# Kernel tuning notes

Measured on AMD Instinct MI355X. Metric: run time of the kernel, lower is better.

## Reference

```python
import jax, jax.numpy as jnp
import numpy as np

B, S, IN_DIM, P_DIM, H = 2, 2048, 1024, 512, 8
HD = P_DIM // H
N_PENTA = 1024
SCALES = (128, 256, 512)
K_NEIGH = max(16, min(int(S * 0.15), 128))  # adaptive window -> 128
SCALE = 1.0 / float(np.sqrt(HD))
EPS = 1e-5


def _ln(x, g, b):
    mu = jnp.mean(x, axis=-1, keepdims=True)
    var = jnp.mean((x - mu) ** 2, axis=-1, keepdims=True)
    return (x - mu) * jax.lax.rsqrt(var + EPS) * g + b


def setup_inputs() -> dict:
    key = jax.random.key(0)
    ks = list(jax.random.split(key, 6 + 2 * len(SCALES)))
    w = lambda k, shp: jax.random.normal(k, shp, jnp.float32) * 0.02
    inp = {
        'sequence_features': jax.random.normal(ks[0], (B, S, IN_DIM), jnp.float32),
        'shared_pentachora': jax.random.normal(ks[1], (N_PENTA, 5, P_DIM), jnp.float32),
        'shared_positions': jax.random.uniform(ks[2], (N_PENTA,), dtype=jnp.float32),
        'proj_W': w(ks[3], (IN_DIM, P_DIM)), 'proj_b': jnp.zeros((P_DIM,), jnp.float32),
        'ln_g': jnp.ones((P_DIM,), jnp.float32), 'ln_b': jnp.zeros((P_DIM,), jnp.float32),
        'qkv_W': w(ks[4], (P_DIM, 3 * P_DIM)), 'qkv_b': jnp.zeros((3 * P_DIM,), jnp.float32),
        'out_W': w(ks[5], (P_DIM, P_DIM)), 'out_b': jnp.zeros((P_DIM,), jnp.float32),
    }
    i = 6
    for s in SCALES:
        inp[f'w1_{s}'] = w(ks[i], (P_DIM, 2 * s)); inp[f'b1_{s}'] = jnp.zeros((2 * s,), jnp.float32)
        inp[f'g_{s}'] = jnp.ones((2 * s,), jnp.float32); inp[f'bb_{s}'] = jnp.zeros((2 * s,), jnp.float32)
        inp[f'w2_{s}'] = w(ks[i + 1], (2 * s, s)); inp[f'b2_{s}'] = jnp.zeros((s,), jnp.float32)
        i += 2
    return inp


def _attend_one(z_b, pos_b, qkv_W, qkv_b, out_W, out_b):
    # z_b: [S, P_DIM], pos_b: [S]
    qkv = (z_b @ qkv_W + qkv_b).reshape(S, 3, H, HD)
    q = jnp.transpose(qkv[:, 0], (1, 0, 2))  # [H, S, HD]
    k = jnp.transpose(qkv[:, 1], (1, 0, 2))
    v = jnp.transpose(qkv[:, 2], (1, 0, 2))
    dist = jnp.abs(pos_b[:, None] - pos_b[None, :])  # [S, S]
    _, routes = jax.lax.top_k(-dist, K_NEIGH)        # [S, K] nearest in Cantor space
    kg = k[:, routes, :]  # [H, S, K, HD] gathered keys
    vg = v[:, routes, :]
    scores = jnp.einsum('hqd,hqkd->hqk', q, kg) * SCALE
    attn = jax.nn.softmax(scores, axis=-1)
    out = jnp.einsum('hqk,hqkd->hqd', attn, vg)
    out = jnp.transpose(out, (1, 0, 2)).reshape(S, P_DIM)
    return out @ out_W + out_b


def reference(sequence_features, shared_pentachora, shared_positions, proj_W, proj_b, ln_g, ln_b, qkv_W, qkv_b, out_W, out_b, w1_128, b1_128, g_128, bb_128, w2_128, b2_128, w1_256, b1_256, g_256, bb_256, w2_256, b2_256, w1_512, b1_512, g_512, bb_512, w2_512, b2_512):
    # centroids from pentachora vertices, L2-normalized
    cent = shared_pentachora.mean(axis=1)
    cent = cent / jnp.clip(jnp.linalg.norm(cent, axis=-1, keepdims=True), 1e-12)
    # input projection -> LN -> GELU -> L2 normalize
    z = jax.nn.gelu(_ln(sequence_features @ proj_W + proj_b, ln_g, ln_b), approximate=False)
    z = z / jnp.clip(jnp.linalg.norm(z, axis=-1, keepdims=True), 1e-12)
    # match to opinion anchors, inherit Cantor positions
    anchor_ids = jnp.argmax(jnp.einsum('bnd,pd->bnp', z, cent), axis=-1)  # [B, S]
    cantor_positions = shared_positions[anchor_ids]  # [B, S]
    # per-sample geometric sparse attention (vmapped over batch)
    z_att = jax.vmap(_attend_one, in_axes=(0, 0, None, None, None, None))(
        z, cantor_positions, qkv_W, qkv_b, out_W, out_b)  # [B, S, P_DIM]
    pooled = z_att.mean(axis=1)  # [B, P_DIM] (no attention mask)
    scale_params = (
        (w1_128, b1_128, g_128, bb_128, w2_128, b2_128),
        (w1_256, b1_256, g_256, bb_256, w2_256, b2_256),
        (w1_512, b1_512, g_512, bb_512, w2_512, b2_512),
    )
    outs = []
    for (w1, b1, g, bb, w2, b2) in scale_params:
        h = jax.nn.gelu(_ln(pooled @ w1 + b1, g, bb), approximate=False)
        outs.append(h @ w2 + b2)
    return jnp.concatenate(outs, axis=-1)  # [B, 128+256+512] concatenated scale opinions
```

## Files before the change

kernel.cpp:

```cpp
#include <hip/hip_runtime.h>
#include <math.h>

#define DEV __device__ __forceinline__

static constexpr int S_LEN  = 2048;
static constexpr int IN_DIM = 1024;
static constexpr int P_DIM  = 512;
static constexpr int NHEAD  = 8;
static constexpr int HD     = 64;
static constexpr int KN     = 128;

typedef __attribute__((ext_vector_type(8))) short bf16x8;
typedef __attribute__((ext_vector_type(4))) float f32x4;

DEV float gelu_exact(float x) {
    return 0.5f * x * (1.0f + erff(x * 0.70710678118654752440f));
}

DEV short bf_hi(float x) {
    unsigned u = __float_as_uint(x);
    unsigned r = (u + 0x7fffu + ((u >> 16) & 1u)) >> 16;
    return (short)r;
}
DEV float bf_f(short h) { return __uint_as_float(((unsigned)(unsigned short)h) << 16); }

DEV float block_reduce_sum(float v, float* sm4) {
    #pragma unroll
    for (int off = 32; off; off >>= 1) v += __shfl_down(v, off, 64);
    int lane = threadIdx.x & 63, w = threadIdx.x >> 6;
    __syncthreads();
    if (lane == 0) sm4[w] = v;
    __syncthreads();
    return sm4[0] + sm4[1] + sm4[2] + sm4[3];
}

__global__ __launch_bounds__(256) void k_cent(const float* __restrict__ penta,
                                              short* __restrict__ ch,
                                              short* __restrict__ cl) {
    int p = blockIdx.x, t = threadIdx.x;
    __shared__ float sm4[4];
    float c0 = 0.f, c1 = 0.f;
    #pragma unroll
    for (int v = 0; v < 5; v++) {
        const float* row = penta + ((long)p * 5 + v) * P_DIM;
        c0 += row[t];
        c1 += row[t + 256];
    }
    c0 /= 5.0f; c1 /= 5.0f;
    float tot = block_reduce_sum(c0 * c0 + c1 * c1, sm4);
    float n = fmaxf(sqrtf(tot), 1e-12f);
    float v0 = c0 / n, v1 = c1 / n;
    short h0 = bf_hi(v0), h1 = bf_hi(v1);
    ch[p * P_DIM + t]       = h0;
    ch[p * P_DIM + t + 256] = h1;
    cl[p * P_DIM + t]       = bf_hi(v0 - bf_f(h0));
    cl[p * P_DIM + t + 256] = bf_hi(v1 - bf_f(h1));
}

template <int K, int N>
__global__ __launch_bounds__(256) void k_wt(const float* __restrict__ W,
                                            short* __restrict__ WTh,
                                            short* __restrict__ WTl) {
    __shared__ float tile[64][65];
    int bk = blockIdx.x, bn = blockIdx.y;
    int t = threadIdx.x;
    int c = t & 63, r4 = t >> 6;
    #pragma unroll
    for (int i = 0; i < 16; i++) {
        int row = r4 + i * 4;
        tile[row][c] = W[(long)(bk * 64 + row) * N + bn * 64 + c];
    }
    __syncthreads();
    #pragma unroll
    for (int i = 0; i < 16; i++) {
        int n = r4 + i * 4;
        float v = tile[c][n];
        short h = bf_hi(v);
        long o = (long)(bn * 64 + n) * K + bk * 64 + c;
        WTh[o] = h;
        WTl[o] = bf_hi(v - bf_f(h));
    }
}

template <int BM, int K, int N, int EPI, bool SPLITA>
__global__ __launch_bounds__(256) void k_mm(const float* __restrict__ Af,
                                            const short* __restrict__ Ash,
                                            const short* __restrict__ Asl,
                                            const short* __restrict__ BTh,
                                            const short* __restrict__ BTl,
                                            const float* __restrict__ bias,
                                            float* __restrict__ C,
                                            unsigned long long* __restrict__ rowkey) {
    constexpr int TI = BM / 32;
    __shared__ short Ah[BM * 40], Al[BM * 40], Bh[128 * 40], Bl[128 * 40];
    int t = threadIdx.x;
    int lane = t & 63, wave = t >> 6;
    int wr = (wave >> 1) * (BM / 2), wc = (wave & 1) * 64;
    int m = lane & 15, quad = lane >> 4;
    int rb = blockIdx.x * BM, cb = blockIdx.y * 128;

    f32x4 acc[TI][4];
    #pragma unroll
    for (int i = 0; i < TI; i++)
        #pragma unroll
        for (int j = 0; j < 4; j++) acc[i][j] = (f32x4){0.f, 0.f, 0.f, 0.f};

    for (int k0 = 0; k0 < K; k0 += 32) {
        __syncthreads();
        if constexpr (SPLITA) {
            #pragma unroll
            for (int ps = 0; ps < BM / 64; ps++) {
                int idx = t + ps * 256;
                int row = idx >> 2, c4 = idx & 3;
                *(float4*)(Ah + row * 40 + c4 * 8) =
                    *(const float4*)(Ash + (long)(rb + row) * K + k0 + c4 * 8);
                *(float4*)(Al + row * 40 + c4 * 8) =
                    *(const float4*)(Asl + (long)(rb + row) * K + k0 + c4 * 8);
            }
        } else {
            #pragma unroll
            for (int ps = 0; ps < BM / 32; ps++) {
                int row = (t >> 3) + ps * 32;
                int seg = t & 7;
                float4 v = *(const float4*)(Af + (long)(rb + row) * K + k0 + seg * 4);
                short h0 = bf_hi(v.x), h1 = bf_hi(v.y), h2 = bf_hi(v.z), h3 = bf_hi(v.w);
                short l0 = bf_hi(v.x - bf_f(h0)), l1 = bf_hi(v.y - bf_f(h1));
                short l2 = bf_hi(v.z - bf_f(h2)), l3 = bf_hi(v.w - bf_f(h3));
                *(short4*)(Ah + row * 40 + seg * 4) = make_short4(h0, h1, h2, h3);
                *(short4*)(Al + row * 40 + seg * 4) = make_short4(l0, l1, l2, l3);
            }
        }
        #pragma unroll
        for (int ps = 0; ps < 2; ps++) {
            int row = (t >> 2) + ps * 64;
            int seg = t & 3;
            *(float4*)(Bh + row * 40 + seg * 8) =
                *(const float4*)(BTh + (long)(cb + row) * K + k0 + seg * 8);
            *(float4*)(Bl + row * 40 + seg * 8) =
                *(const float4*)(BTl + (long)(cb + row) * K + k0 + seg * 8);
        }
        __syncthreads();

        bf16x8 ah[TI], al[TI], bh[4], bl[4];
        #pragma unroll
        for (int i = 0; i < TI; i++) {
            ah[i] = *(const bf16x8*)(Ah + (wr + i * 16 + m) * 40 + quad * 8);
            al[i] = *(const bf16x8*)(Al + (wr + i * 16 + m) * 40 + quad * 8);
        }
        #pragma unroll
        for (int j = 0; j < 4; j++) {
            bh[j] = *(const bf16x8*)(Bh + (wc + j * 16 + m) * 40 + quad * 8);
            bl[j] = *(const bf16x8*)(Bl + (wc + j * 16 + m) * 40 + quad * 8);
        }
        #pragma unroll
        for (int i = 0; i < TI; i++)
            #pragma unroll
            for (int j = 0; j < 4; j++) {
                acc[i][j] = __builtin_amdgcn_mfma_f32_16x16x32_bf16(ah[i], bh[j], acc[i][j], 0, 0, 0);
                acc[i][j] = __builtin_amdgcn_mfma_f32_16x16x32_bf16(ah[i], bl[j], acc[i][j], 0, 0, 0);
                acc[i][j] = __builtin_amdgcn_mfma_f32_16x16x32_bf16(al[i], bh[j], acc[i][j], 0, 0, 0);
            }
    }

    if (EPI == 0) {
        #pragma unroll
        for (int i = 0; i < TI; i++) {
            int gr0 = rb + wr + i * 16 + quad * 4;
            #pragma unroll
            for (int j = 0; j < 4; j++) {
                int gc = cb + wc + j * 16 + m;
                float bv = bias[gc];
                #pragma unroll
                for (int r = 0; r < 4; r++)
                    C[(long)(gr0 + r) * N + gc] = acc[i][j][r] + bv;
            }
        }
    } else {
        #pragma unroll
        for (int i = 0; i < TI; i++) {
            #pragma unroll
            for (int r = 0; r < 4; r++) {
                int gr = rb + wr + i * 16 + quad * 4 + r;
                float bv = acc[i][0][r];
                int bp = cb + wc + m;
                #pragma unroll
                for (int j = 1; j < 4; j++) {
                    float v = acc[i][j][r];
                    int p = cb + wc + j * 16 + m;
                    if (v > bv) { bv = v; bp = p; }
                }
                #pragma unroll
                for (int off = 1; off < 16; off <<= 1) {
                    float ov = __shfl_xor(bv, off, 64);
                    int op = __shfl_xor(bp, off, 64);
                    if (ov > bv || (ov == bv && op < bp)) { bv = ov; bp = op; }
                }
                if (m == 0) {
                    unsigned u = __float_as_uint(bv);
                    u = (u & 0x80000000u) ? ~u : (u | 0x80000000u);
                    unsigned long long key =
                        ((unsigned long long)u << 32) | (unsigned)(0xFFFFFFFFu - (unsigned)bp);
                    atomicMax(&rowkey[gr], key);
                }
            }
        }
    }
}

__global__ __launch_bounds__(256) void k_ln_gelu_norm(const float* __restrict__ Zin,
                                                      const float* __restrict__ g,
                                                      const float* __restrict__ b,
                                                      short* __restrict__ z_h,
                                                      short* __restrict__ z_l) {
    long row = blockIdx.x;
    int t = threadIdx.x;
    __shared__ float sm4[4];
    float x0 = Zin[row * P_DIM + t], x1 = Zin[row * P_DIM + t + 256];
    float mu = block_reduce_sum(x0 + x1, sm4) * (1.0f / P_DIM);
    float d0 = x0 - mu, d1 = x1 - mu;
    float var = block_reduce_sum(d0 * d0 + d1 * d1, sm4) * (1.0f / P_DIM);
    float rs = 1.0f / sqrtf(var + 1e-5f);
    float y0 = gelu_exact(d0 * rs * g[t] + b[t]);
    float y1 = gelu_exact(d1 * rs * g[t + 256] + b[t + 256]);
    float nn = block_reduce_sum(y0 * y0 + y1 * y1, sm4);
    float n = fmaxf(sqrtf(nn), 1e-12f);
    float v0 = y0 / n, v1 = y1 / n;
    short h0 = bf_hi(v0), h1 = bf_hi(v1);
    z_h[row * P_DIM + t]       = h0;
    z_h[row * P_DIM + t + 256] = h1;
    z_l[row * P_DIM + t]       = bf_hi(v0 - bf_f(h0));
    z_l[row * P_DIM + t + 256] = bf_hi(v1 - bf_f(h1));
}

__global__ __launch_bounds__(256) void k_sort(const unsigned long long* __restrict__ rowkey,
                                              const float* __restrict__ spos,
                                              int* __restrict__ order,
                                              float* __restrict__ pos_srt) {
    int b = blockIdx.x, t = threadIdx.x;
    __shared__ unsigned long long key[2048];
    for (int u = 0; u < 8; u++) {
        int i = t + u * 256;
        unsigned p = 0xFFFFFFFFu - (unsigned)(rowkey[b * 2048 + i] & 0xFFFFFFFFull);
        float pv = spos[p];
        key[i] = (((unsigned long long)__float_as_uint(pv)) << 32) | (unsigned)i;
    }
    __syncthreads();
    for (int k = 2; k <= 2048; k <<= 1) {
        for (int j = k >> 1; j > 0; j >>= 1) {
            for (int u = 0; u < 8; u++) {
                int i = t + u * 256;
                int l = i ^ j;
                if (l > i) {
                    bool up = ((i & k) == 0);
                    unsigned long long a = key[i], c = key[l];
                    if ((a > c) == up) { key[i] = c; key[l] = a; }
                }
            }
            __syncthreads();
        }
    }
    for (int u = 0; u < 8; u++) {
        int r = t + u * 256;
        unsigned long long kk = key[r];
        order[b * 2048 + r]   = (int)(kk & 0xffffffffu);
        pos_srt[b * 2048 + r] = __uint_as_float((unsigned)(kk >> 32));
    }
}

__global__ __launch_bounds__(256) void k_routes(const float* __restrict__ pos_srt,
                                                const int* __restrict__ order,
                                                unsigned long long* __restrict__ bmG,
                                                uint2* __restrict__ bounds) {
    int blk = blockIdx.x;
    int b = blk >> 9;
    int t = threadIdx.x;
    int lane = t & 63, wave = t >> 6;
    int r = (blk & 511) * 4 + wave;
    __shared__ float ps[2048];
    __shared__ unsigned short tk[2048];
    for (int u = 0; u < 8; u++) {
        int i = t + u * 256;
        ps[i] = pos_srt[b * 2048 + i];
        tk[i] = (unsigned short)order[b * 2048 + i];
    }
    __syncthreads();

    float pi = ps[r];
    float T = 3e38f;
    #pragma unroll
    for (int a2 = 0; a2 < 2; a2++) {
        int a = lane + a2 * 64;
        int jl = r - a, jr = r + 127 - a;
        if (jl >= 0 && jr <= 2047) {
            float dl = (a > 0)   ? (pi - ps[jl]) : 0.f;
            float dr = (a < 127) ? (ps[jr] - pi) : 0.f;
            T = fminf(T, fmaxf(dl, dr));
        }
    }
    #pragma unroll
    for (int off = 1; off < 64; off <<= 1) T = fminf(T, __shfl_xor(T, off, 64));

    int lo = 0, hi = r;
    while (lo < hi) { int mid = (lo + hi) >> 1; if (pi - ps[mid] <= T) hi = mid; else lo = mid + 1; }
    int mn = lo;
    lo = r; hi = 2047;
    while (lo < hi) { int mid = (lo + hi + 1) >> 1; if (ps[mid] - pi <= T) lo = mid; else hi = mid - 1; }
    int mx = lo;
    int Ls, Rs;
    if (T > 0.f) {
        lo = 0; hi = r;
        while (lo < hi) { int mid = (lo + hi) >> 1; if (pi - ps[mid] < T) hi = mid; else lo = mid + 1; }
        Ls = lo;
        lo = r; hi = 2047;
        while (lo < hi) { int mid = (lo + hi + 1) >> 1; if (ps[mid] - pi < T) lo = mid; else hi = mid - 1; }
        Rs = lo;
    } else { Ls = r + 1; Rs = r - 1; }

    int cnt_strict = (Rs >= Ls) ? (Rs - Ls + 1) : 0;
    int need = 128 - cnt_strict;
    int l0a, l0b, r0a, r0b;
    if (cnt_strict > 0) { l0a = mn; l0b = Ls - 1; r0a = Rs + 1; r0b = mx; }
    else                { l0a = mn; l0b = mx;     r0a = 1;      r0b = 0; }
    int nL = (l0b >= l0a) ? (l0b - l0a + 1) : 0;
    int nR = (r0b >= r0a) ? (r0b - r0a + 1) : 0;
    int tiecount = nL + nR;

    int X = 65535;
    if (need < tiecount) {
        int lo2 = 0, hi2 = 2047;
        while (lo2 < hi2) {
            int mid = (lo2 + hi2) >> 1;
            int cnt = 0;
            for (int e = lane; e < tiecount; e += 64) {
                int j = (e < nL) ? (l0a + e) : (r0a + e - nL);
                cnt += (tk[j] <= mid) ? 1 : 0;
            }
            #pragma unroll
            for (int off = 1; off < 64; off <<= 1) cnt += __shfl_xor(cnt, off, 64);
            if (cnt >= need) hi2 = mid; else lo2 = mid + 1;
        }
        X = lo2;
    }

    int qlo_loc = 1 << 30, qhi_loc = -1;
    if (lane < 32) {
        unsigned long long bits = 0;
        int j0 = lane << 6, j1 = j0 + 63;
        if (cnt_strict > 0) {
            int a0 = max(Ls, j0), a1 = min(Rs, j1);
            if (a0 <= a1) {
                int s = a0 - j0, e = a1 - j0;
                unsigned long long msk = (e - s == 63) ? ~0ull
                                       : (((1ull << (e - s + 1)) - 1) << s);
                bits |= msk;
            }
        }
        int a0 = max(l0a, j0), a1 = min(l0b, j1);
        for (int j = a0; j <= a1; j++) if (tk[j] <= X) bits |= 1ull << (j - j0);
        a0 = max(r0a, j0); a1 = min(r0b, j1);
        for (int j = a0; j <= a1; j++) if (tk[j] <= X) bits |= 1ull << (j - j0);
        if (bits) {
            qlo_loc = j0 + __builtin_ctzll(bits);
            qhi_loc = j0 + 63 - __builtin_clzll(bits);
        }
        bmG[((long)(b * 2048 + r)) * 32 + lane] = bits;
    }
    #pragma unroll
    for (int off = 1; off < 64; off <<= 1) {
        qlo_loc = min(qlo_loc, __shfl_xor(qlo_loc, off, 64));
        qhi_loc = max(qhi_loc, __shfl_xor(qhi_loc, off, 64));
    }
    if (lane == 0)
        bounds[b * 2048 + r] = make_uint2((unsigned)qlo_loc, (unsigned)qhi_loc);
}

__global__ __launch_bounds__(256) void k_attn(const float* __restrict__ qkv,
                                              const int* __restrict__ order,
                                              const unsigned long long* __restrict__ bmG,
                                              const uint2* __restrict__ bounds,
                                              short* __restrict__ attn_h,
                                              short* __restrict__ attn_l) {
    __shared__ __align__(16) char smem[72320];
    short* Khi = (short*)smem;
    short* Klo = (short*)(smem + 17408);
    short* Vt  = (short*)(smem + 34816);
    short* Pt  = (short*)(smem + 57344);
    unsigned short* cm = (unsigned short*)(smem + 67584);
    int* sh_tok = (int*)(smem + 71680);
    int* sh_lohi = (int*)(smem + 71744);
    float2* ml = (float2*)(smem + 71752);
    float* Opart = (float*)smem;

    int gb = blockIdx.x;
    int b  = gb >> 9;
    int qg = (gb >> 2) & 127;
    int hp = gb & 3;
    int h0 = hp * 2;
    int r0 = qg * 16;
    int t = threadIdx.x;
    int lane = t & 63, wave = t >> 6;
    int rh = wave & 1, hs = wave >> 1;
    int key = lane & 15, quad = lane >> 4;

    const float4* qkvF4 = (const float4*)qkv;

    if (t < 16) sh_tok[t] = order[b * 2048 + r0 + t];
    if (t == 0) { sh_lohi[0] = 1 << 30; sh_lohi[1] = 0; }
    #pragma unroll
    for (int u = 0; u < 8; u++) {
        int e = t + u * 256;
        int c = e >> 4, q = e & 15;
        cm[c * 16 + q] = (unsigned short)(
            (bmG[((long)(b * 2048 + r0 + q)) * 32 + (c >> 2)] >> ((c & 3) * 16)) & 0xFFFF);
    }
    __syncthreads();
    if (t < 16) {
        uint2 bd = bounds[b * 2048 + r0 + t];
        atomicMin(&sh_lohi[0], (int)bd.x);
        atomicMax(&sh_lohi[1], (int)bd.y);
    }

    bf16x8 qh[2], ql[2];
    {
        long tq = (long)(b * 2048 + sh_tok[key]) * 384;
        #pragma unroll
        for (int ks = 0; ks < 2; ks++) {
            float4 v0 = qkvF4[tq + (h0 + hs) * 16 + ks * 8 + quad * 2];
            float4 v1 = qkvF4[tq + (h0 + hs) * 16 + ks * 8 + quad * 2 + 1];
            float vv[8] = {v0.x, v0.y, v0.z, v0.w, v1.x, v1.y, v1.z, v1.w};
            #pragma unroll
            for (int j = 0; j < 8; j++) {
                short hb = bf_hi(vv[j]);
                qh[ks][j] = hb;
                ql[ks][j] = bf_hi(vv[j] - bf_f(hb));
            }
        }
    }
    __syncthreads();
    int lo = sh_lohi[0] & ~63, hi = sh_lohi[1] + 1;

    float mrow[4], lrow[4];
    f32x4 Ont[4];
    #pragma unroll
    for (int r = 0; r < 4; r++) { mrow[r] = -1e30f; lrow[r] = 0.f; }
    #pragma unroll
    for (int nt = 0; nt < 4; nt++) Ont[nt] = (f32x4){0.f, 0.f, 0.f, 0.f};

    short* PtH = Pt + wave * 1280;
    short* PtL = PtH + 640;

    for (int c0 = lo; c0 < hi; c0 += 64) {
        __syncthreads();
        #pragma unroll
        for (int u = 0; u < 8; u++) {
            int idx = t + u * 256;
            int rl = idx >> 5, f4p = idx & 31;
            int rank = c0 + rl;
            int tok = order[b * 2048 + min(rank, 2047)];
            float4 v = qkvF4[(long)(b * 2048 + tok) * 384 + 128 + h0 * 16 + f4p];
            short h0s = bf_hi(v.x), h1s = bf_hi(v.y), h2s = bf_hi(v.z), h3s = bf_hi(v.w);
            *(short4*)(Khi + rl * 136 + f4p * 4) = make_short4(h0s, h1s, h2s, h3s);
            *(short4*)(Klo + rl * 136 + f4p * 4) =
                make_short4(bf_hi(v.x - bf_f(h0s)), bf_hi(v.y - bf_f(h1s)),
                            bf_hi(v.z - bf_f(h2s)), bf_hi(v.w - bf_f(h3s)));
        }
        {
            int rq = t & 15;
            int dp = t >> 4;
            float4 va[4][2];
            #pragma unroll
            for (int i = 0; i < 4; i++) {
                int rank = c0 + rq * 4 + i;
                int tok = order[b * 2048 + min(rank, 2047)];
                long base = (long)(b * 2048 + tok) * 384 + 256 + h0 * 16 + dp * 2;
                va[i][0] = qkvF4[base];
                va[i][1] = qkvF4[base + 1];
            }
            #pragma unroll
            for (int j2 = 0; j2 < 2; j2++)
                #pragma unroll
                for (int c = 0; c < 4; c++) {
                    const float* f0 = (const float*)&va[0][j2];
                    const float* f1 = (const float*)&va[1][j2];
                    const float* f2 = (const float*)&va[2][j2];
                    const float* f3 = (const float*)&va[3][j2];
                    *(short4*)(Vt + (dp * 8 + j2 * 4 + c) * 88 + rq * 4) =
                        make_short4(bf_hi(f0[c]), bf_hi(f1[c]), bf_hi(f2[c]), bf_hi(f3[c]));
                }
        }
        __syncthreads();

        int cb = c0 + rh * 32;
        if (cb >= hi) continue;
        int ch0 = cb >> 4;
        unsigned long long m0 = *(const unsigned long long*)(cm + ch0 * 16 + quad * 4);
        unsigned long long m1 = (ch0 + 1 < 128)
            ? *(const unsigned long long*)(cm + (ch0 + 1) * 16 + quad * 4) : 0ull;
        if (!__any((m0 | m1) != 0ull)) continue;

        f32x4 S0 = (f32x4){0.f,0.f,0.f,0.f}, S1 = (f32x4){0.f,0.f,0.f,0.f};
        #pragma unroll
        for (int ks = 0; ks < 2; ks++) {
            const short* kb0 = Khi + (rh * 32 + key) * 136 + hs * 64 + ks * 32 + quad * 8;
            const short* kl0 = Klo + (rh * 32 + key) * 136 + hs * 64 + ks * 32 + quad * 8;
            const short* kb1 = kb0 + 16 * 136;
            const short* kl1 = kl0 + 16 * 136;
            bf16x8 b0h = *(const bf16x8*)kb0, b0l = *(const bf16x8*)kl0;
            bf16x8 b1h = *(const bf16x8*)kb1, b1l = *(const bf16x8*)kl1;
            S0 = __builtin_amdgcn_mfma_f32_16x16x32_bf16(qh[ks], b0h, S0, 0, 0, 0);
            S0 = __builtin_amdgcn_mfma_f32_16x16x32_bf16(qh[ks], b0l, S0, 0, 0, 0);
            S0 = __builtin_amdgcn_mfma_f32_16x16x32_bf16(ql[ks], b0h, S0, 0, 0, 0);
            S1 = __builtin_amdgcn_mfma_f32_16x16x32_bf16(qh[ks], b1h, S1, 0, 0, 0);
            S1 = __builtin_amdgcn_mfma_f32_16x16x32_bf16(qh[ks], b1l, S1, 0, 0, 0);
            S1 = __builtin_amdgcn_mfma_f32_16x16x32_bf16(ql[ks], b1h, S1, 0, 0, 0);
        }
        float s0[4], s1[4], p0[4], p1[4];
        unsigned bit0[4], bit1[4];
        #pragma unroll
        for (int r = 0; r < 4; r++) {
            bit0[r] = (unsigned)((m0 >> (r * 16 + key)) & 1);
            bit1[r] = (unsigned)((m1 >> (r * 16 + key)) & 1);
            s0[r] = bit0[r] ? S0[r] * 0.125f : -1e30f;
            s1[r] = bit1[r] ? S1[r] * 0.125f : -1e30f;
        }
        #pragma unroll
        for (int r = 0; r < 4; r++) {
            float cmax = fmaxf(s0[r], s1[r]);
            cmax = fmaxf(cmax, __shfl_xor(cmax, 1, 64));
            cmax = fmaxf(cmax, __shfl_xor(cmax, 2, 64));
            cmax = fmaxf(cmax, __shfl_xor(cmax, 4, 64));
            cmax = fmaxf(cmax, __shfl_xor(cmax, 8, 64));
            float mn = fmaxf(mrow[r], cmax);
            float alpha = __expf(mrow[r] - mn);
            mrow[r] = mn;
            p0[r] = bit0[r] ? __expf(s0[r] - mn) : 0.f;
            p1[r] = bit1[r] ? __expf(s1[r] - mn) : 0.f;
            float rs = p0[r] + p1[r];
            rs += __shfl_xor(rs, 1, 64);
            rs += __shfl_xor(rs, 2, 64);
            rs += __shfl_xor(rs, 4, 64);
            rs += __shfl_xor(rs, 8, 64);
            lrow[r] = lrow[r] * alpha + rs;
            #pragma unroll
            for (int nt = 0; nt < 4; nt++) Ont[nt][r] *= alpha;
        }
        #pragma unroll
        for (int r = 0; r < 4; r++) {
            short ha = bf_hi(p0[r]);
            PtH[(quad * 4 + r) * 40 + key] = ha;
            PtL[(quad * 4 + r) * 40 + key] = bf_hi(p0[r] - bf_f(ha));
            short hb = bf_hi(p1[r]);
            PtH[(quad * 4 + r) * 40 + 16 + key] = hb;
            PtL[(quad * 4 + r) * 40 + 16 + key] = bf_hi(p1[r] - bf_f(hb));
        }
        bf16x8 pfh = *(const bf16x8*)(PtH + key * 40 + quad * 8);
        bf16x8 pfl = *(const bf16x8*)(PtL + key * 40 + quad * 8);
        #pragma unroll
        for (int nt = 0; nt < 4; nt++) {
            bf16x8 vf = *(const bf16x8*)(Vt + (hs * 64 + nt * 16 + key) * 88
                                         + rh * 32 + quad * 8);
            Ont[nt] = __builtin_amdgcn_mfma_f32_16x16x32_bf16(pfh, vf, Ont[nt], 0, 0, 0);
            Ont[nt] = __builtin_amdgcn_mfma_f32_16x16x32_bf16(pfl, vf, Ont[nt], 0, 0, 0);
        }
    }

    if (key == 0) {
        #pragma unroll
        for (int r = 0; r < 4; r++)
            ml[(rh * 2 + hs) * 16 + quad * 4 + r] = make_float2(mrow[r], lrow[r]);
    }
    __syncthreads();
    #pragma unroll
    for (int nt = 0; nt < 4; nt++)
        #pragma unroll
        for (int r = 0; r < 4; r++)
            Opart[rh * 2048 + (quad * 4 + r) * 128 + hs * 64 + nt * 16 + key] = Ont[nt][r];
    __syncthreads();

    {
        int q = t >> 4, hs2 = (t >> 3) & 1, ds = t & 7;
        float2 a = ml[(0 * 2 + hs2) * 16 + q];
        float2 c = ml[(1 * 2 + hs2) * 16 + q];
        float M = fmaxf(a.x, c.x);
        float w0 = __expf(a.x - M), w1 = __expf(c.x - M);
        float denom = a.y * w0 + c.y * w1;
        float inv = 1.0f / fmaxf(denom, 1e-37f);
        long off = (long)(b * 2048 + sh_tok[q]) * P_DIM + (h0 + hs2) * HD + ds * 8;
        short hsv[8], lsv[8];
        #pragma unroll
        for (int j = 0; j < 8; j++) {
            int d = hs2 * 64 + ds * 8 + j;
            float o = (Opart[q * 128 + d] * w0 + Opart[2048 + q * 128 + d] * w1) * inv;
            hsv[j] = bf_hi(o);
            lsv[j] = bf_hi(o - bf_f(hsv[j]));
        }
        *(short4*)(attn_h + off)     = make_short4(hsv[0], hsv[1], hsv[2], hsv[3]);
        *(short4*)(attn_h + off + 4) = make_short4(hsv[4], hsv[5], hsv[6], hsv[7]);
        *(short4*)(attn_l + off)     = make_short4(lsv[0], lsv[1], lsv[2], lsv[3]);
        *(short4*)(attn_l + off + 4) = make_short4(lsv[4], lsv[5], lsv[6], lsv[7]);
    }
}

__global__ __launch_bounds__(256) void k_pool(const float* __restrict__ zatt,
                                              float* __restrict__ pooled) {
    int b = blockIdx.y, chunk = blockIdx.x, t = threadIdx.x;
    float a0 = 0.f, a1 = 0.f;
    for (int s = 0; s < 16; s++) {
        long row = ((long)b * S_LEN + chunk * 16 + s) * P_DIM;
        a0 += zatt[row + t];
        a1 += zatt[row + t + 256];
    }
    atomicAdd(&pooled[b * P_DIM + t], a0);
    atomicAdd(&pooled[b * P_DIM + t + 256], a1);
}

__global__ __launch_bounds__(256) void k_exp_fc1(const float* __restrict__ pooled,
                                                 const float* __restrict__ w1_0, const float* __restrict__ b1_0,
                                                 const float* __restrict__ w1_1, const float* __restrict__ b1_1,
                                                 const float* __restrict__ w1_2, const float* __restrict__ b1_2,
                                                 float* __restrict__ h) {
    int t = threadIdx.x, b = blockIdx.y;
    int c = blockIdx.x * 256 + t;
    __shared__ float pl[P_DIM];
    pl[t]       = pooled[b * P_DIM + t]       * (1.0f / S_LEN);
    pl[t + 256] = pooled[b * P_DIM + t + 256] * (1.0f / S_LEN);
    __syncthreads();

    const float* wp; const float* bp; int s2, j;
    if (c < 256)      { wp = w1_0; bp = b1_0; s2 = 256;  j = c; }
    else if (c < 768) { wp = w1_1; bp = b1_1; s2 = 512;  j = c - 256; }
    else              { wp = w1_2; bp = b1_2; s2 = 1024; j = c - 768; }

    const float* p = wp + j;
    float acc = 0.f;
    #pragma unroll 16
    for (int k = 0; k < P_DIM; k++) {
        acc = fmaf(pl[k], *p, acc);
        p += s2;
    }
    h[(long)b * 1792 + c] = acc + bp[j];
}

__global__ __launch_bounds__(256) void k_exp_ln(float* __restrict__ h,
                                                const float* __restrict__ g0, const float* __restrict__ bb0,
                                                const float* __restrict__ g1, const float* __restrict__ bb1,
                                                const float* __restrict__ g2, const float* __restrict__ bb2) {
    int e = blockIdx.x, b = blockIdx.y, t = threadIdx.x;
    __shared__ float sm4[4];
    const int offs[3] = {0, 256, 768};
    const int ns[3]   = {256, 512, 1024};
    const float* gs[3]  = {g0, g1, g2};
    const float* bbs[3] = {bb0, bb1, bb2};
    int n = ns[e];
    float* hp = h + (long)b * 1792 + offs[e];
    const float* g = gs[e]; const float* bb = bbs[e];

    float x[4];
    float loc = 0.f;
    for (int u = 0; u < 4; u++) {
        int j = t + u * 256;
        x[u] = (j < n) ? hp[j] : 0.f;
        loc += x[u];
    }
    float mu = block_reduce_sum(loc, sm4) / (float)n;
    loc = 0.f;
    for (int u = 0; u < 4; u++) {
        int j = t + u * 256;
        if (j < n) { float d = x[u] - mu; loc += d * d; }
    }
    float var = block_reduce_sum(loc, sm4) / (float)n;
    float rs = 1.0f / sqrtf(var + 1e-5f);
    for (int u = 0; u < 4; u++) {
        int j = t + u * 256;
        if (j < n) hp[j] = gelu_exact((x[u] - mu) * rs * g[j] + bb[j]);
    }
}

__global__ __launch_bounds__(256) void k_exp_fc2(const float* __restrict__ h,
                                                 const float* __restrict__ w2_0, const float* __restrict__ b2_0,
                                                 const float* __restrict__ w2_1, const float* __restrict__ b2_1,
                                                 const float* __restrict__ w2_2, const float* __restrict__ b2_2,
                                                 float* __restrict__ out) {
    int t = threadIdx.x, b = blockIdx.y;
    int c = blockIdx.x * 256 + t;
    __shared__ float hs[1792];
    for (int u = 0; u < 7; u++) hs[t + u * 256] = h[(long)b * 1792 + t + u * 256];
    __syncthreads();
    if (c >= 896) return;

    const float* wp; const float* bp; int s2, sN, j, off_h;
    if (c < 128)      { wp = w2_0; bp = b2_0; s2 = 256;  sN = 128; j = c;       off_h = 0; }
    else if (c < 384) { wp = w2_1; bp = b2_1; s2 = 512;  sN = 256; j = c - 128; off_h = 256; }
    else              { wp = w2_2; bp = b2_2; s2 = 1024; sN = 512; j = c - 384; off_h = 768; }

    const float* p = wp + j;
    const float* hh = hs + off_h;
    float acc = 0.f;
    #pragma unroll 16
    for (int k = 0; k < s2; k++) {
        acc = fmaf(hh[k], *p, acc);
        p += sN;
    }
    out[b * 896 + c] = acc + bp[j];
}

extern "C" void kernel_launch(void* const* d_in, const int* in_sizes, int n_in,
                              void* d_out, int out_size, void* d_ws, size_t ws_size,
                              hipStream_t stream) {
    const float* seq   = (const float*)d_in[0];
    const float* penta = (const float*)d_in[1];
    const float* spos  = (const float*)d_in[2];
    const float* projW = (const float*)d_in[3];
    const float* projb = (const float*)d_in[4];
    const float* lng   = (const float*)d_in[5];
    const float* lnb   = (const float*)d_in[6];
    const float* qkvW  = (const float*)d_in[7];
    const float* qkvb  = (const float*)d_in[8];
    const float* outW  = (const float*)d_in[9];
    const float* outb  = (const float*)d_in[10];

    float* ws      = (float*)d_ws;
    float* z_pre   = ws;
    short* z_h     = (short*)(z_pre + 2097152);
    short* z_l     = z_h + 2097152;
    float* qkv     = (float*)(z_l + 2097152);
    float* pos     = qkv + 6291456;
    float* pooled  = pos + 4096;
    float* hbuf    = pooled + 1024;
    unsigned long long* rowkey = (unsigned long long*)(hbuf + 4096);
    float* pos_srt = (float*)(rowkey + 4096);
    int*   order   = (int*)(pos_srt + 4096);
    uint2* bounds  = (uint2*)(order + 4096);
    unsigned long long* bmG = (unsigned long long*)(bounds + 4096);
    short* cent_h  = (short*)(bmG + 131072);
    short* cent_l  = cent_h + 524288;
    short* pjWT_h  = cent_l + 524288;
    short* pjWT_l  = pjWT_h + 524288;
    short* qkWT_h  = pjWT_l + 524288;
    short* qkWT_l  = qkWT_h + 786432;
    short* owWT_h  = qkWT_l + 786432;
    short* owWT_l  = owWT_h + 262144;
    short* attn_h  = z_h;
    short* attn_l  = z_l;
    float* zatt    = z_pre;

    k_cent<<<1024, 256, 0, stream>>>(penta, cent_h, cent_l);
    { dim3 g(16, 8);  k_wt<IN_DIM, P_DIM><<<g, 256, 0, stream>>>(projW, pjWT_h, pjWT_l); }
    { dim3 g(8, 24);  k_wt<P_DIM, 3 * P_DIM><<<g, 256, 0, stream>>>(qkvW, qkWT_h, qkWT_l); }
    { dim3 g(8, 8);   k_wt<P_DIM, P_DIM><<<g, 256, 0, stream>>>(outW, owWT_h, owWT_l); }

    { dim3 g(64, 4);  k_mm<64, IN_DIM, P_DIM, 0, false><<<g, 256, 0, stream>>>(
          seq, nullptr, nullptr, pjWT_h, pjWT_l, projb, z_pre, nullptr); }
    k_ln_gelu_norm<<<4096, 256, 0, stream>>>(z_pre, lng, lnb, z_h, z_l);

    hipMemsetAsync(rowkey, 0, 4096 * sizeof(unsigned long long), stream);
    { dim3 g(64, 8);  k_mm<64, P_DIM, 1024, 1, true><<<g, 256, 0, stream>>>(
          nullptr, z_h, z_l, cent_h, cent_l, nullptr, nullptr, rowkey); }
    k_sort<<<2, 256, 0, stream>>>(rowkey, spos, order, pos_srt);

    { dim3 g(64, 12); k_mm<64, P_DIM, 3 * P_DIM, 0, true><<<g, 256, 0, stream>>>(
          nullptr, z_h, z_l, qkWT_h, qkWT_l, qkvb, qkv, nullptr); }
    k_routes<<<1024, 256, 0, stream>>>(pos_srt, order, bmG, bounds);
    k_attn<<<1024, 256, 0, stream>>>(qkv, order, bmG, bounds, attn_h, attn_l);
    { dim3 g(64, 4);  k_mm<64, P_DIM, P_DIM, 0, true><<<g, 256, 0, stream>>>(
          nullptr, attn_h, attn_l, owWT_h, owWT_l, outb, zatt, nullptr); }

    hipMemsetAsync(pooled, 0, 1024 * sizeof(float), stream);
    { dim3 pg(128, 2); k_pool<<<pg, 256, 0, stream>>>(zatt, pooled); }

    dim3 g1(7, 2);
    k_exp_fc1<<<g1, 256, 0, stream>>>(pooled,
        (const float*)d_in[11], (const float*)d_in[12],
        (const float*)d_in[17], (const float*)d_in[18],
        (const float*)d_in[23], (const float*)d_in[24], hbuf);
    dim3 g2(3, 2);
    k_exp_ln<<<g2, 256, 0, stream>>>(hbuf,
        (const float*)d_in[13], (const float*)d_in[14],
        (const float*)d_in[19], (const float*)d_in[20],
        (const float*)d_in[25], (const float*)d_in[26]);
    dim3 g3(4, 2);
    k_exp_fc2<<<g3, 256, 0, stream>>>(hbuf,
        (const float*)d_in[15], (const float*)d_in[16],
        (const float*)d_in[21], (const float*)d_in[22],
        (const float*)d_in[27], (const float*)d_in[28], (float*)d_out);
}
```

Before: 403.4 us.

## Pre-sort and pre-split K/V into global bf16 layouts before attention

Two new kernels gather K and V in sorted Cantor order once. K is split into bf16 hi/lo halves and V is transposed to bf16 in global scratch buffers. The attention kernel then reads MFMA fragments straight from global memory instead of re-gathering and converting K/V into LDS for every query block. This removes redundant conversion work and two syncthreads per chunk, and shrinks LDS use to allow more occupancy. The cost is extra kernel launches, scratch traffic, and uncoalesced global fragment loads inside the inner loop that rely on cache hits.

```diff
diff --git a/kernel.cpp b/kernel.cpp
--- a/kernel.cpp
+++ b/kernel.cpp
@@ -374,22 +374,75 @@
         bounds[b * 2048 + r] = make_uint2((unsigned)qlo_loc, (unsigned)qhi_loc);
 }
 
+__global__ __launch_bounds__(256) void k_kprep(const float* __restrict__ qkv,
+                                               const int* __restrict__ order,
+                                               short* __restrict__ Ks_h,
+                                               short* __restrict__ Ks_l) {
+    int b = blockIdx.y;
+    int t = threadIdx.x;
+    int lr = t >> 5;
+    int seg = t & 31;
+    int rank = blockIdx.x * 8 + lr;
+    int tok = order[b * 2048 + rank];
+    const float4* src = (const float4*)qkv + (long)(b * 2048 + tok) * 384 + 128 + seg * 4;
+    long dsto = (long)(b * 2048 + rank) * 512 + seg * 16;
+    #pragma unroll
+    for (int u = 0; u < 4; u++) {
+        float4 v = src[u];
+        short h0 = bf_hi(v.x), h1 = bf_hi(v.y), h2 = bf_hi(v.z), h3 = bf_hi(v.w);
+        *(short4*)(Ks_h + dsto + u * 4) = make_short4(h0, h1, h2, h3);
+        *(short4*)(Ks_l + dsto + u * 4) =
+            make_short4(bf_hi(v.x - bf_f(h0)), bf_hi(v.y - bf_f(h1)),
+                        bf_hi(v.z - bf_f(h2)), bf_hi(v.w - bf_f(h3)));
+    }
+}
+
+__global__ __launch_bounds__(256) void k_vprep(const float* __restrict__ qkv,
+                                               const int* __restrict__ order,
+                                               short* __restrict__ Vt_h) {
+    __shared__ short tile[64][72];
+    int rt = blockIdx.x, dt = blockIdx.y, b = blockIdx.z;
+    int t = threadIdx.x;
+    int lr = t >> 2;
+    int q4 = t & 3;
+    int tok = order[b * 2048 + rt * 64 + lr];
+    const float4* src = (const float4*)qkv + (long)(b * 2048 + tok) * 384 + 256 + dt * 16;
+    #pragma unroll
+    for (int u = 0; u < 4; u++) {
+        float4 v = src[q4 + u * 4];
+        int d0 = (q4 + u * 4) * 4;
+        tile[d0 + 0][lr] = bf_hi(v.x);
+        tile[d0 + 1][lr] = bf_hi(v.y);
+        tile[d0 + 2][lr] = bf_hi(v.z);
+        tile[d0 + 3][lr] = bf_hi(v.w);
+    }
+    __syncthreads();
+    int d = t >> 2, c4 = t & 3;
+    long o = ((long)(b * 512 + dt * 64 + d)) * 2048 + rt * 64 + c4 * 16;
+    #pragma unroll
+    for (int j = 0; j < 4; j++)
+        *(short4*)(Vt_h + o + j * 4) = make_short4(tile[d][c4 * 16 + j * 4 + 0],
+                                                   tile[d][c4 * 16 + j * 4 + 1],
+                                                   tile[d][c4 * 16 + j * 4 + 2],
+                                                   tile[d][c4 * 16 + j * 4 + 3]);
+}
+
 __global__ __launch_bounds__(256) void k_attn(const float* __restrict__ qkv,
                                               const int* __restrict__ order,
                                               const unsigned long long* __restrict__ bmG,
                                               const uint2* __restrict__ bounds,
+                                              const short* __restrict__ Ks_h,
+                                              const short* __restrict__ Ks_l,
+                                              const short* __restrict__ Vt_h,
                                               short* __restrict__ attn_h,
                                               short* __restrict__ attn_l) {
-    __shared__ __align__(16) char smem[72320];
-    short* Khi = (short*)smem;
-    short* Klo = (short*)(smem + 17408);
-    short* Vt  = (short*)(smem + 34816);
-    short* Pt  = (short*)(smem + 57344);
-    unsigned short* cm = (unsigned short*)(smem + 67584);
-    int* sh_tok = (int*)(smem + 71680);
-    int* sh_lohi = (int*)(smem + 71744);
-    float2* ml = (float2*)(smem + 71752);
+    __shared__ __align__(16) char smem[17024];
+    short* Pt = (short*)smem;
+    unsigned short* cm = (unsigned short*)(smem + 10240);
     float* Opart = (float*)smem;
+    float2* ml = (float2*)(smem + 16384);
+    int* sh_tok = (int*)(smem + 16896);
+    int* sh_lohi = (int*)(smem + 16960);
 
     int gb = blockIdx.x;
     int b  = gb >> 9;
@@ -449,47 +502,11 @@
     short* PtH = Pt + wave * 1280;
     short* PtL = PtH + 640;
 
+    int hd = h0 + hs;
+    long kbase = ((long)b * 2048) * 512 + hd * 64 + quad * 8;
+    long vbase = ((long)(b * 512 + hd * 64 + key)) * 2048;
+
     for (int c0 = lo; c0 < hi; c0 += 64) {
-        __syncthreads();
-        #pragma unroll
-        for (int u = 0; u < 8; u++) {
-            int idx = t + u * 256;
-            int rl = idx >> 5, f4p = idx & 31;
-            int rank = c0 + rl;
-            int tok = order[b * 2048 + min(rank, 2047)];
-            float4 v = qkvF4[(long)(b * 2048 + tok) * 384 + 128 + h0 * 16 + f4p];
-            short h0s = bf_hi(v.x), h1s = bf_hi(v.y), h2s = bf_hi(v.z), h3s = bf_hi(v.w);
-            *(short4*)(Khi + rl * 136 + f4p * 4) = make_short4(h0s, h1s, h2s, h3s);
-            *(short4*)(Klo + rl * 136 + f4p * 4) =
-                make_short4(bf_hi(v.x - bf_f(h0s)), bf_hi(v.y - bf_f(h1s)),
-                            bf_hi(v.z - bf_f(h2s)), bf_hi(v.w - bf_f(h3s)));
-        }
-        {
-            int rq = t & 15;
-            int dp = t >> 4;
-            float4 va[4][2];
-            #pragma unroll
-            for (int i = 0; i < 4; i++) {
-                int rank = c0 + rq * 4 + i;
-                int tok = order[b * 2048 + min(rank, 2047)];
-                long base = (long)(b * 2048 + tok) * 384 + 256 + h0 * 16 + dp * 2;
-                va[i][0] = qkvF4[base];
-                va[i][1] = qkvF4[base + 1];
-            }
-            #pragma unroll
-            for (int j2 = 0; j2 < 2; j2++)
-                #pragma unroll
-                for (int c = 0; c < 4; c++) {
-                    const float* f0 = (const float*)&va[0][j2];
-                    const float* f1 = (const float*)&va[1][j2];
-                    const float* f2 = (const float*)&va[2][j2];
-                    const float* f3 = (const float*)&va[3][j2];
-                    *(short4*)(Vt + (dp * 8 + j2 * 4 + c) * 88 + rq * 4) =
-                        make_short4(bf_hi(f0[c]), bf_hi(f1[c]), bf_hi(f2[c]), bf_hi(f3[c]));
-                }
-        }
-        __syncthreads();
-
         int cb = c0 + rh * 32;
         if (cb >= hi) continue;
         int ch0 = cb >> 4;
@@ -498,15 +515,16 @@
             ? *(const unsigned long long*)(cm + (ch0 + 1) * 16 + quad * 4) : 0ull;
         if (!__any((m0 | m1) != 0ull)) continue;
 
+        long kr0 = kbase + (long)(cb + key) * 512;
+        long kr1 = kbase + (long)(cb + 16 + key) * 512;
+
         f32x4 S0 = (f32x4){0.f,0.f,0.f,0.f}, S1 = (f32x4){0.f,0.f,0.f,0.f};
         #pragma unroll
         for (int ks = 0; ks < 2; ks++) {
-            const short* kb0 = Khi + (rh * 32 + key) * 136 + hs * 64 + ks * 32 + quad * 8;
-            const short* kl0 = Klo + (rh * 32 + key) * 136 + hs * 64 + ks * 32 + quad * 8;
-            const short* kb1 = kb0 + 16 * 136;
-            const short* kl1 = kl0 + 16 * 136;
-            bf16x8 b0h = *(const bf16x8*)kb0, b0l = *(const bf16x8*)kl0;
-            bf16x8 b1h = *(const bf16x8*)kb1, b1l = *(const bf16x8*)kl1;
+            bf16x8 b0h = *(const bf16x8*)(Ks_h + kr0 + ks * 32);
+            bf16x8 b0l = *(const bf16x8*)(Ks_l + kr0 + ks * 32);
+            bf16x8 b1h = *(const bf16x8*)(Ks_h + kr1 + ks * 32);
+            bf16x8 b1l = *(const bf16x8*)(Ks_l + kr1 + ks * 32);
             S0 = __builtin_amdgcn_mfma_f32_16x16x32_bf16(qh[ks], b0h, S0, 0, 0, 0);
             S0 = __builtin_amdgcn_mfma_f32_16x16x32_bf16(qh[ks], b0l, S0, 0, 0, 0);
             S0 = __builtin_amdgcn_mfma_f32_16x16x32_bf16(ql[ks], b0h, S0, 0, 0, 0);
@@ -557,8 +575,8 @@
         bf16x8 pfl = *(const bf16x8*)(PtL + key * 40 + quad * 8);
         #pragma unroll
         for (int nt = 0; nt < 4; nt++) {
-            bf16x8 vf = *(const bf16x8*)(Vt + (hs * 64 + nt * 16 + key) * 88
-                                         + rh * 32 + quad * 8);
+            bf16x8 vf = *(const bf16x8*)(Vt_h + vbase + (long)nt * 16 * 2048
+                                         + cb + quad * 8);
             Ont[nt] = __builtin_amdgcn_mfma_f32_16x16x32_bf16(pfh, vf, Ont[nt], 0, 0, 0);
             Ont[nt] = __builtin_amdgcn_mfma_f32_16x16x32_bf16(pfl, vf, Ont[nt], 0, 0, 0);
         }
@@ -744,6 +762,10 @@
     short* attn_l  = z_l;
     float* zatt    = z_pre;
 
+    short* Ks_h = (short*)z_pre;
+    short* Ks_l = Ks_h + 2097152;
+    short* Vt_h = cent_h;
+
     k_cent<<<1024, 256, 0, stream>>>(penta, cent_h, cent_l);
     { dim3 g(16, 8);  k_wt<IN_DIM, P_DIM><<<g, 256, 0, stream>>>(projW, pjWT_h, pjWT_l); }
     { dim3 g(8, 24);  k_wt<P_DIM, 3 * P_DIM><<<g, 256, 0, stream>>>(qkvW, qkWT_h, qkWT_l); }
@@ -761,7 +783,10 @@
     { dim3 g(64, 12); k_mm<64, P_DIM, 3 * P_DIM, 0, true><<<g, 256, 0, stream>>>(
           nullptr, z_h, z_l, qkWT_h, qkWT_l, qkvb, qkv, nullptr); }
     k_routes<<<1024, 256, 0, stream>>>(pos_srt, order, bmG, bounds);
-    k_attn<<<1024, 256, 0, stream>>>(qkv, order, bmG, bounds, attn_h, attn_l);
+    { dim3 g(256, 2); k_kprep<<<g, 256, 0, stream>>>(qkv, order, Ks_h, Ks_l); }
+    { dim3 g(32, 8, 2); k_vprep<<<g, 256, 0, stream>>>(qkv, order, Vt_h); }
+    k_attn<<<1024, 256, 0, stream>>>(qkv, order, bmG, bounds,
+                                     Ks_h, Ks_l, Vt_h, attn_h, attn_l);
     { dim3 g(64, 4);  k_mm<64, P_DIM, P_DIM, 0, true><<<g, 256, 0, stream>>>(
           nullptr, attn_h, attn_l, owWT_h, owWT_l, outb, zatt, nullptr); }
 
```

Result: no change. 401.8 us (-0.4%).
